# Kernel tuning notes

Hardware: AMD Instinct MI355X
Metric: run time of the kernel (lower is better)

## Reference

```python
import jax, jax.numpy as jnp
import numpy as np

HEAD_DIM = 64
K = 3              # kernel_size
DILATION = 1
SCALE = HEAD_DIM ** (-0.5)
PAD = DILATION * (K - 1) // 2


def setup_inputs() -> dict:
    key = jax.random.key(0)
    kq, kk, kv = jax.random.split(key, 3)
    shape = (8, 512, 56, 56)  # B, d, H, W
    return {
        "q": jax.random.normal(kq, shape, dtype=jnp.float32),
        "k": jax.random.normal(kk, shape, dtype=jnp.float32),
        "v": jax.random.normal(kv, shape, dtype=jnp.float32),
    }


def _unfold(x, B, h, H, W):
    # torch nn.Unfold(kernel=K, dilation=1, padding=PAD, stride=1):
    # output [B, d*K*K, H*W] with (channel, kh, kw) channel-major ordering,
    # which matches lax.conv_general_dilated_patches output layout.
    p = jax.lax.conv_general_dilated_patches(
        x, (K, K), (1, 1), ((PAD, PAD), (PAD, PAD)),
        rhs_dilation=(DILATION, DILATION),
        dimension_numbers=("NCHW", "OIHW", "NCHW"),
    )  # [B, d*K*K, H, W]
    return p.reshape(B, h, HEAD_DIM, K * K, H * W)


def reference(q, k, v):
    B, d, H, W = q.shape
    h = d // HEAD_DIM  # number of heads
    # q -> [B, h, HW, head_dim]
    qr = q.reshape(B, h, HEAD_DIM, H * W).transpose(0, 1, 3, 2)
    ku = _unfold(k, B, h, H, W)  # [B, h, hd, K*K, HW]
    vu = _unfold(v, B, h, H, W)  # [B, h, hd, K*K, HW]
    # per-pixel local attention over the K*K window
    attn = jnp.einsum("bhpc,bhckp->bhpk", qr, ku) * SCALE  # [B,h,HW,K*K]
    attn = jax.nn.softmax(attn, axis=-1)
    out = jnp.einsum("bhpk,bhckp->bhpc", attn, vu)  # [B,h,HW,hd]
    # -> [B, HW, h, hd] -> [B, H, W, d]
    return out.transpose(0, 2, 1, 3).reshape(B, H, W, d)
```

## Files before the change

kernel.cpp:

```cpp
#include <hip/hip_runtime.h>


namespace {

constexpr int HD = 64, HH = 56, WW = 56, HW = HH * WW;
constexpr int CS = HW, DTOT = 512;
constexpr float SCALE = 0.125f;
constexpr int NP   = HH / 2;
constexpr int TSTR = 36;

__device__ __forceinline__ float tapL(float v) {
  int i = __float_as_int(v);
  return __int_as_float(__builtin_amdgcn_update_dpp(i, i, 0x138, 0xF, 0xF, false));
}
__device__ __forceinline__ float tapR(float v) {
  int i = __float_as_int(v);
  return __int_as_float(__builtin_amdgcn_update_dpp(i, i, 0x130, 0xF, 0xF, false));
}

__global__ __launch_bounds__(64, 2)
void adda_fwd(const float* __restrict__ qg, const float* __restrict__ kg,
              const float* __restrict__ vg, float* __restrict__ outg) {
  __shared__ float tbuf[128 * TSTR];

  int wg = (int)blockIdx.x;
  const int nwg = (int)gridDim.x;
  if ((nwg & 7) == 0) wg = (wg & 7) * (nwg >> 3) + (wg >> 3);

  const int pair = wg % NP;
  const int bh   = wg / NP;
  const int l    = (int)threadIdx.x;
  const int y    = pair * 2;
  const int x    = l < WW ? l : WW - 1;

  const long base = (long)bh * HD * HW;
  const int gy0 = (y > 0) ? y - 1 : 0;
  const int gy3 = (y + 2 < HH) ? y + 2 : HH - 1;

  const float* __restrict__ qp0 = qg + base + (long)y * WW + x;
  const float* __restrict__ qp1 = qg + base + (long)(y + 1) * WW + x;
  const float* __restrict__ k0p = kg + base + (long)gy0 * WW + x;
  const float* __restrict__ k1p = kg + base + (long)y * WW + x;
  const float* __restrict__ k2p = kg + base + (long)(y + 1) * WW + x;
  const float* __restrict__ k3p = kg + base + (long)gy3 * WW + x;
  const float* __restrict__ v0p = vg + base + (long)gy0 * WW + x;
  const float* __restrict__ v1p = vg + base + (long)y * WW + x;
  const float* __restrict__ v2p = vg + base + (long)(y + 1) * WW + x;
  const float* __restrict__ v3p = vg + base + (long)gy3 * WW + x;

  float lg[18];
#pragma unroll
  for (int n = 0; n < 18; ++n) lg[n] = 0.f;

  float q0A[8], q1A[8], a0A[8], a1A[8], a2A[8], a3A[8];
  float q0B[8], q1B[8], a0B[8], a1B[8], a2B[8], a3B[8];

#define LOADK(S, cb)                                    \
  _Pragma("unroll") for (int i = 0; i < 8; ++i) {       \
    q0##S[i] = qp0[((cb) + i) * CS];                    \
    q1##S[i] = qp1[((cb) + i) * CS];                    \
    a0##S[i] = k0p[((cb) + i) * CS];                    \
    a1##S[i] = k1p[((cb) + i) * CS];                    \
    a2##S[i] = k2p[((cb) + i) * CS];                    \
    a3##S[i] = k3p[((cb) + i) * CS];                    \
  }
#define CONSK(S)                                        \
  _Pragma("unroll") for (int i = 0; i < 8; ++i) {       \
    const float t0l = tapL(a0##S[i]), t0r = tapR(a0##S[i]); \
    const float t1l = tapL(a1##S[i]), t1r = tapR(a1##S[i]); \
    const float t2l = tapL(a2##S[i]), t2r = tapR(a2##S[i]); \
    const float t3l = tapL(a3##S[i]), t3r = tapR(a3##S[i]); \
    const float q0 = q0##S[i], q1 = q1##S[i];           \
    lg[0]  = fmaf(q0, t0l,      lg[0]);                 \
    lg[1]  = fmaf(q0, a0##S[i], lg[1]);                 \
    lg[2]  = fmaf(q0, t0r,      lg[2]);                 \
    lg[3]  = fmaf(q0, t1l,      lg[3]);                 \
    lg[4]  = fmaf(q0, a1##S[i], lg[4]);                 \
    lg[5]  = fmaf(q0, t1r,      lg[5]);                 \
    lg[6]  = fmaf(q0, t2l,      lg[6]);                 \
    lg[7]  = fmaf(q0, a2##S[i], lg[7]);                 \
    lg[8]  = fmaf(q0, t2r,      lg[8]);                 \
    lg[9]  = fmaf(q1, t1l,      lg[9]);                 \
    lg[10] = fmaf(q1, a1##S[i], lg[10]);                \
    lg[11] = fmaf(q1, t1r,      lg[11]);                \
    lg[12] = fmaf(q1, t2l,      lg[12]);                \
    lg[13] = fmaf(q1, a2##S[i], lg[13]);                \
    lg[14] = fmaf(q1, t2r,      lg[14]);                \
    lg[15] = fmaf(q1, t3l,      lg[15]);                \
    lg[16] = fmaf(q1, a3##S[i], lg[16]);                \
    lg[17] = fmaf(q1, t3r,      lg[17]);                \
  }

  LOADK(A, 0);
  LOADK(B, 8);  CONSK(A);
  LOADK(A, 16); CONSK(B);
  LOADK(B, 24); CONSK(A);
  LOADK(A, 32); CONSK(B);
  LOADK(B, 40); CONSK(A);
  LOADK(A, 48); CONSK(B);
  LOADK(B, 56); CONSK(A);

  float b0A[8], b1A[8], b2A[8], b3A[8];
  float b0B[8], b1B[8], b2B[8], b3B[8];
#define LOADV(S, cb)                                    \
  _Pragma("unroll") for (int i = 0; i < 8; ++i) {       \
    b0##S[i] = v0p[((cb) + i) * CS];                    \
    b1##S[i] = v1p[((cb) + i) * CS];                    \
    b2##S[i] = v2p[((cb) + i) * CS];                    \
    b3##S[i] = v3p[((cb) + i) * CS];                    \
  }
  LOADV(A, 0);
  CONSK(B);

  const bool okl = x > 0, okr = x < WW - 1;
  const bool okt0 = y > 0;
  const bool okb1 = (y + 2) < HH;
  const bool ok[18] = {
    okt0 && okl, okt0, okt0 && okr,
    okl,         true, okr,
    okl,         true, okr,
    okl,         true, okr,
    okl,         true, okr,
    okb1 && okl, okb1, okb1 && okr};
  float w[18];
#pragma unroll
  for (int e = 0; e < 2; ++e) {
    float mx = 0.f;
#pragma unroll
    for (int n = 0; n < 9; ++n) {
      w[e * 9 + n] = ok[e * 9 + n] ? lg[e * 9 + n] * SCALE : 0.f;
      mx = fmaxf(mx, w[e * 9 + n]);
    }
    float sum = 0.f;
#pragma unroll
    for (int n = 0; n < 9; ++n) { w[e * 9 + n] = __expf(w[e * 9 + n] - mx); sum += w[e * 9 + n]; }
    const float inv = 1.f / sum;
#pragma unroll
    for (int n = 0; n < 9; ++n)
      w[e * 9 + n] = ok[e * 9 + n] ? w[e * 9 + n] * inv : 0.f;
  }

  float* __restrict__ ob =
      outg + ((long)(bh >> 3) * HW + (long)y * WW) * DTOT + (bh & 7) * HD;

#define CONSV(S, sl)                                    \
  {                                                     \
    float o0[8], o1[8];                                 \
    _Pragma("unroll") for (int i = 0; i < 8; ++i) {     \
      const float t0l = tapL(b0##S[i]), t0r = tapR(b0##S[i]); \
      const float t1l = tapL(b1##S[i]), t1r = tapR(b1##S[i]); \
      const float t2l = tapL(b2##S[i]), t2r = tapR(b2##S[i]); \
      const float t3l = tapL(b3##S[i]), t3r = tapR(b3##S[i]); \
      float a = w[0] * t0l;                             \
      a = fmaf(w[1], b0##S[i], a);                      \
      a = fmaf(w[2], t0r, a);                           \
      a = fmaf(w[3], t1l, a);                           \
      a = fmaf(w[4], b1##S[i], a);                      \
      a = fmaf(w[5], t1r, a);                           \
      a = fmaf(w[6], t2l, a);                           \
      a = fmaf(w[7], b2##S[i], a);                      \
      a = fmaf(w[8], t2r, a);                           \
      o0[i] = a;                                        \
      float c = w[9] * t1l;                             \
      c = fmaf(w[10], b1##S[i], c);                     \
      c = fmaf(w[11], t1r, c);                          \
      c = fmaf(w[12], t2l, c);                          \
      c = fmaf(w[13], b2##S[i], c);                     \
      c = fmaf(w[14], t2r, c);                          \
      c = fmaf(w[15], t3l, c);                          \
      c = fmaf(w[16], b3##S[i], c);                     \
      c = fmaf(w[17], t3r, c);                          \
      o1[i] = c;                                        \
    }                                                   \
    *(float4*)&tbuf[l * TSTR + (sl) * 8]            = make_float4(o0[0], o0[1], o0[2], o0[3]); \
    *(float4*)&tbuf[l * TSTR + (sl) * 8 + 4]        = make_float4(o0[4], o0[5], o0[6], o0[7]); \
    *(float4*)&tbuf[(64 + l) * TSTR + (sl) * 8]     = make_float4(o1[0], o1[1], o1[2], o1[3]); \
    *(float4*)&tbuf[(64 + l) * TSTR + (sl) * 8 + 4] = make_float4(o1[4], o1[5], o1[6], o1[7]); \
  }
#define READOUT(ch0)                                    \
  _Pragma("unroll") for (int r = 0; r < 14; ++r) {      \
    const int g = r * 64 + l;                           \
    const int pxl = g >> 3, slot = g & 7;               \
    const int lrow = pxl + ((pxl >= 56) ? 8 : 0);       \
    const float4 tv = *(const float4*)&tbuf[lrow * TSTR + slot * 4]; \
    *(float4*)(ob + (long)pxl * DTOT + (ch0) + slot * 4) = tv;      \
  }

  LOADV(B, 8);  CONSV(A, 0);
  LOADV(A, 16); CONSV(B, 1);
  LOADV(B, 24); CONSV(A, 2);
  LOADV(A, 32); CONSV(B, 3);
  LOADV(B, 40); READOUT(0);
  CONSV(A, 0);
  LOADV(A, 48); CONSV(B, 1);
  LOADV(B, 56); CONSV(A, 2);
                CONSV(B, 3);
  READOUT(32);

#undef LOADK
#undef CONSK
#undef LOADV
#undef CONSV
#undef READOUT
}

}

extern "C" void kernel_launch(void* const* d_in, const int* in_sizes, int n_in,
                              void* d_out, int out_size, void* d_ws, size_t ws_size,
                              hipStream_t stream) {
  const float* q = (const float*)d_in[0];
  const float* k = (const float*)d_in[1];
  const float* v = (const float*)d_in[2];
  float* out = (float*)d_out;

  const int BH = in_sizes[0] / (HD * HW);
  dim3 grid(BH * NP);
  adda_fwd<<<grid, 64, 0, stream>>>(q, k, v, out);
}
```

Before: 33.81 us.

## Switch to triple-buffered 4-channel load pipeline for K and V stages

Replaces the double-buffered 8-channel register pipeline with three 4-channel buffers, so two chunks of loads stay in flight while the third is consumed. This aims to hide global-load latency better at roughly the same register footprint. Stores to the LDS transpose buffer become one float4 per row per chunk. The risks are that the finer chunks add more wait points, and that the compiler's scheduling or register allocation changes at 2 waves per SIMD.

After: 33.60 us, median of 2. No clear change (-0.6%).

```diff
diff --git a/kernel.cpp b/kernel.cpp
--- a/kernel.cpp
+++ b/kernel.cpp
@@ -52,11 +52,12 @@
 #pragma unroll
   for (int n = 0; n < 18; ++n) lg[n] = 0.f;
 
-  float q0A[8], q1A[8], a0A[8], a1A[8], a2A[8], a3A[8];
-  float q0B[8], q1B[8], a0B[8], a1B[8], a2B[8], a3B[8];
+  float q0A[4], q1A[4], a0A[4], a1A[4], a2A[4], a3A[4];
+  float q0B[4], q1B[4], a0B[4], a1B[4], a2B[4], a3B[4];
+  float q0C[4], q1C[4], a0C[4], a1C[4], a2C[4], a3C[4];
 
 #define LOADK(S, cb)                                    \
-  _Pragma("unroll") for (int i = 0; i < 8; ++i) {       \
+  _Pragma("unroll") for (int i = 0; i < 4; ++i) {       \
     q0##S[i] = qp0[((cb) + i) * CS];                    \
     q1##S[i] = qp1[((cb) + i) * CS];                    \
     a0##S[i] = k0p[((cb) + i) * CS];                    \
@@ -65,7 +66,7 @@
     a3##S[i] = k3p[((cb) + i) * CS];                    \
   }
 #define CONSK(S)                                        \
-  _Pragma("unroll") for (int i = 0; i < 8; ++i) {       \
+  _Pragma("unroll") for (int i = 0; i < 4; ++i) {       \
     const float t0l = tapL(a0##S[i]), t0r = tapR(a0##S[i]); \
     const float t1l = tapL(a1##S[i]), t1r = tapR(a1##S[i]); \
     const float t2l = tapL(a2##S[i]), t2r = tapR(a2##S[i]); \
@@ -91,26 +92,34 @@
     lg[17] = fmaf(q1, t3r,      lg[17]);                \
   }
 
-  LOADK(A, 0);
-  LOADK(B, 8);  CONSK(A);
-  LOADK(A, 16); CONSK(B);
-  LOADK(B, 24); CONSK(A);
-  LOADK(A, 32); CONSK(B);
-  LOADK(B, 40); CONSK(A);
-  LOADK(A, 48); CONSK(B);
-  LOADK(B, 56); CONSK(A);
-
-  float b0A[8], b1A[8], b2A[8], b3A[8];
-  float b0B[8], b1B[8], b2B[8], b3B[8];
+  float b0A[4], b1A[4], b2A[4], b3A[4];
+  float b0B[4], b1B[4], b2B[4], b3B[4];
+  float b0C[4], b1C[4], b2C[4], b3C[4];
 #define LOADV(S, cb)                                    \
-  _Pragma("unroll") for (int i = 0; i < 8; ++i) {       \
+  _Pragma("unroll") for (int i = 0; i < 4; ++i) {       \
     b0##S[i] = v0p[((cb) + i) * CS];                    \
     b1##S[i] = v1p[((cb) + i) * CS];                    \
     b2##S[i] = v2p[((cb) + i) * CS];                    \
     b3##S[i] = v3p[((cb) + i) * CS];                    \
   }
-  LOADV(A, 0);
-  CONSK(B);
+
+  LOADK(A, 0); LOADK(B, 4); LOADK(C, 8);
+  CONSK(A); LOADK(A, 12);
+  CONSK(B); LOADK(B, 16);
+  CONSK(C); LOADK(C, 20);
+  CONSK(A); LOADK(A, 24);
+  CONSK(B); LOADK(B, 28);
+  CONSK(C); LOADK(C, 32);
+  CONSK(A); LOADK(A, 36);
+  CONSK(B); LOADK(B, 40);
+  CONSK(C); LOADK(C, 44);
+  CONSK(A); LOADK(A, 48);
+  CONSK(B); LOADK(B, 52);
+  CONSK(C); LOADK(C, 56);
+  CONSK(A); LOADK(A, 60);
+  CONSK(B); LOADV(A, 0);
+  CONSK(C); LOADV(B, 4);
+  CONSK(A); LOADV(C, 8);
 
   const bool okl = x > 0, okr = x < WW - 1;
   const bool okt0 = y > 0;
@@ -145,8 +154,8 @@
 
 #define CONSV(S, sl)                                    \
   {                                                     \
-    float o0[8], o1[8];                                 \
-    _Pragma("unroll") for (int i = 0; i < 8; ++i) {     \
+    float o0[4], o1[4];                                 \
+    _Pragma("unroll") for (int i = 0; i < 4; ++i) {     \
       const float t0l = tapL(b0##S[i]), t0r = tapR(b0##S[i]); \
       const float t1l = tapL(b1##S[i]), t1r = tapR(b1##S[i]); \
       const float t2l = tapL(b2##S[i]), t2r = tapR(b2##S[i]); \
@@ -172,10 +181,10 @@
       c = fmaf(w[17], t3r, c);                          \
       o1[i] = c;                                        \
     }                                                   \
-    *(float4*)&tbuf[l * TSTR + (sl) * 8]            = make_float4(o0[0], o0[1], o0[2], o0[3]); \
-    *(float4*)&tbuf[l * TSTR + (sl) * 8 + 4]        = make_float4(o0[4], o0[5], o0[6], o0[7]); \
-    *(float4*)&tbuf[(64 + l) * TSTR + (sl) * 8]     = make_float4(o1[0], o1[1], o1[2], o1[3]); \
-    *(float4*)&tbuf[(64 + l) * TSTR + (sl) * 8 + 4] = make_float4(o1[4], o1[5], o1[6], o1[7]); \
+    *(float4*)&tbuf[l * TSTR + (sl) * 4] =              \
+        make_float4(o0[0], o0[1], o0[2], o0[3]);        \
+    *(float4*)&tbuf[(64 + l) * TSTR + (sl) * 4] =       \
+        make_float4(o1[0], o1[1], o1[2], o1[3]);        \
   }
 #define READOUT(ch0)                                    \
   _Pragma("unroll") for (int r = 0; r < 14; ++r) {      \
@@ -186,15 +195,23 @@
     *(float4*)(ob + (long)pxl * DTOT + (ch0) + slot * 4) = tv;      \
   }
 
-  LOADV(B, 8);  CONSV(A, 0);
-  LOADV(A, 16); CONSV(B, 1);
-  LOADV(B, 24); CONSV(A, 2);
-  LOADV(A, 32); CONSV(B, 3);
-  LOADV(B, 40); READOUT(0);
-  CONSV(A, 0);
-  LOADV(A, 48); CONSV(B, 1);
-  LOADV(B, 56); CONSV(A, 2);
-                CONSV(B, 3);
+  CONSV(A, 0); LOADV(A, 12);
+  CONSV(B, 1); LOADV(B, 16);
+  CONSV(C, 2); LOADV(C, 20);
+  CONSV(A, 3); LOADV(A, 24);
+  CONSV(B, 4); LOADV(B, 28);
+  CONSV(C, 5); LOADV(C, 32);
+  CONSV(A, 6); LOADV(A, 36);
+  CONSV(B, 7); LOADV(B, 40);
+  READOUT(0);
+  CONSV(C, 0); LOADV(C, 44);
+  CONSV(A, 1); LOADV(A, 48);
+  CONSV(B, 2); LOADV(B, 52);
+  CONSV(C, 3); LOADV(C, 56);
+  CONSV(A, 4); LOADV(A, 60);
+  CONSV(B, 5);
+  CONSV(C, 6);
+  CONSV(A, 7);
   READOUT(32);
 
 #undef LOADK
```

## Split work across two waves: channel-split QK logits, row-split PV output

Applied to the files above, without the earlier changes.

Each workgroup now runs two wavefronts. For the logits, each wave accumulates partial dot products over half of the 64 channels and the halves are combined through shared memory with barriers. For the output, each wave handles one of the two output rows and loads only three V rows, which removes the duplicated second-row FMA chain per wave. This doubles thread-level parallelism and lowers per-wave register pressure, in exchange for an LDS reduction, two __syncthreads, and some redundant V row loads across the two waves.

Result: slower. 44.27 us (+30.9%).

```diff
diff --git a/kernel.cpp b/kernel.cpp
--- a/kernel.cpp
+++ b/kernel.cpp
@@ -18,10 +18,10 @@
   return __int_as_float(__builtin_amdgcn_update_dpp(i, i, 0x130, 0xF, 0xF, false));
 }
 
-__global__ __launch_bounds__(64, 2)
+__global__ __launch_bounds__(128, 4)
 void adda_fwd(const float* __restrict__ qg, const float* __restrict__ kg,
               const float* __restrict__ vg, float* __restrict__ outg) {
-  __shared__ float tbuf[128 * TSTR];
+  __shared__ float tbuf[2 * 64 * TSTR];
 
   int wg = (int)blockIdx.x;
   const int nwg = (int)gridDim.x;
@@ -29,24 +29,29 @@
 
   const int pair = wg % NP;
   const int bh   = wg / NP;
-  const int l    = (int)threadIdx.x;
+  const int l    = (int)threadIdx.x & 63;
+  const int wv   = (int)threadIdx.x >> 6;
   const int y    = pair * 2;
+  const int yr   = y + wv;
   const int x    = l < WW ? l : WW - 1;
 
-  const long base = (long)bh * HD * HW;
+  const long base  = (long)bh * HD * HW;
+  const long cbase = base + (long)(wv * 32) * CS;
   const int gy0 = (y > 0) ? y - 1 : 0;
   const int gy3 = (y + 2 < HH) ? y + 2 : HH - 1;
 
-  const float* __restrict__ qp0 = qg + base + (long)y * WW + x;
-  const float* __restrict__ qp1 = qg + base + (long)(y + 1) * WW + x;
-  const float* __restrict__ k0p = kg + base + (long)gy0 * WW + x;
-  const float* __restrict__ k1p = kg + base + (long)y * WW + x;
-  const float* __restrict__ k2p = kg + base + (long)(y + 1) * WW + x;
-  const float* __restrict__ k3p = kg + base + (long)gy3 * WW + x;
-  const float* __restrict__ v0p = vg + base + (long)gy0 * WW + x;
-  const float* __restrict__ v1p = vg + base + (long)y * WW + x;
-  const float* __restrict__ v2p = vg + base + (long)(y + 1) * WW + x;
-  const float* __restrict__ v3p = vg + base + (long)gy3 * WW + x;
+  const float* __restrict__ qp0 = qg + cbase + (long)y * WW + x;
+  const float* __restrict__ qp1 = qg + cbase + (long)(y + 1) * WW + x;
+  const float* __restrict__ k0p = kg + cbase + (long)gy0 * WW + x;
+  const float* __restrict__ k1p = kg + cbase + (long)y * WW + x;
+  const float* __restrict__ k2p = kg + cbase + (long)(y + 1) * WW + x;
+  const float* __restrict__ k3p = kg + cbase + (long)gy3 * WW + x;
+
+  const int vy0 = (yr > 0) ? yr - 1 : 0;
+  const int vy2 = (yr + 1 < HH) ? yr + 1 : HH - 1;
+  const float* __restrict__ v0p = vg + base + (long)vy0 * WW + x;
+  const float* __restrict__ v1p = vg + base + (long)yr * WW + x;
+  const float* __restrict__ v2p = vg + base + (long)vy2 * WW + x;
 
   float lg[18];
 #pragma unroll
@@ -91,66 +96,67 @@
     lg[17] = fmaf(q1, t3r,      lg[17]);                \
   }
 
-  LOADK(A, 0);
-  LOADK(B, 8);  CONSK(A);
-  LOADK(A, 16); CONSK(B);
-  LOADK(B, 24); CONSK(A);
-  LOADK(A, 32); CONSK(B);
-  LOADK(B, 40); CONSK(A);
-  LOADK(A, 48); CONSK(B);
-  LOADK(B, 56); CONSK(A);
-
-  float b0A[8], b1A[8], b2A[8], b3A[8];
-  float b0B[8], b1B[8], b2B[8], b3B[8];
+  float b0A[8], b1A[8], b2A[8];
+  float b0B[8], b1B[8], b2B[8];
 #define LOADV(S, cb)                                    \
   _Pragma("unroll") for (int i = 0; i < 8; ++i) {       \
     b0##S[i] = v0p[((cb) + i) * CS];                    \
     b1##S[i] = v1p[((cb) + i) * CS];                    \
     b2##S[i] = v2p[((cb) + i) * CS];                    \
-    b3##S[i] = v3p[((cb) + i) * CS];                    \
-  }
+  }
+
+  LOADK(A, 0);
+  LOADK(B, 8);  CONSK(A);
+  LOADK(A, 16); CONSK(B);
+  LOADK(B, 24); CONSK(A);
+                CONSK(B);
   LOADV(A, 0);
-  CONSK(B);
+  LOADV(B, 8);
+
+  {
+    float* outbox = &tbuf[wv * 2304];
+    const int src = wv ? 0 : 9;
+#pragma unroll
+    for (int n = 0; n < 9; ++n) outbox[n * 64 + l] = lg[src + n];
+  }
+  __syncthreads();
+  {
+    const float* inbox = &tbuf[(wv ^ 1) * 2304];
+    const int dst = wv ? 9 : 0;
+#pragma unroll
+    for (int n = 0; n < 9; ++n) lg[dst + n] += inbox[n * 64 + l];
+  }
+  __syncthreads();
 
   const bool okl = x > 0, okr = x < WW - 1;
-  const bool okt0 = y > 0;
-  const bool okb1 = (y + 2) < HH;
-  const bool ok[18] = {
-    okt0 && okl, okt0, okt0 && okr,
-    okl,         true, okr,
-    okl,         true, okr,
-    okl,         true, okr,
-    okl,         true, okr,
-    okb1 && okl, okb1, okb1 && okr};
-  float w[18];
-#pragma unroll
-  for (int e = 0; e < 2; ++e) {
-    float mx = 0.f;
-#pragma unroll
-    for (int n = 0; n < 9; ++n) {
-      w[e * 9 + n] = ok[e * 9 + n] ? lg[e * 9 + n] * SCALE : 0.f;
-      mx = fmaxf(mx, w[e * 9 + n]);
-    }
-    float sum = 0.f;
-#pragma unroll
-    for (int n = 0; n < 9; ++n) { w[e * 9 + n] = __expf(w[e * 9 + n] - mx); sum += w[e * 9 + n]; }
-    const float inv = 1.f / sum;
-#pragma unroll
-    for (int n = 0; n < 9; ++n)
-      w[e * 9 + n] = ok[e * 9 + n] ? w[e * 9 + n] * inv : 0.f;
-  }
-
+  const bool vt = wv ? true : (y > 0);
+  const bool vb = wv ? (y + 2 < HH) : true;
+  const bool ok[9] = {vt && okl, vt, vt && okr,
+                      okl,       true, okr,
+                      vb && okl, vb, vb && okr};
+  const int lo = wv * 9;
+  float w[9];
+  float mx = 0.f;
+#pragma unroll
+  for (int n = 0; n < 9; ++n) { w[n] = ok[n] ? lg[lo + n] * SCALE : 0.f; mx = fmaxf(mx, w[n]); }
+  float sum = 0.f;
+#pragma unroll
+  for (int n = 0; n < 9; ++n) { w[n] = __expf(w[n] - mx); sum += w[n]; }
+  const float inv = 1.f / sum;
+#pragma unroll
+  for (int n = 0; n < 9; ++n) w[n] = ok[n] ? w[n] * inv : 0.f;
+
+  float* __restrict__ tw = &tbuf[wv * 64 * TSTR];
   float* __restrict__ ob =
-      outg + ((long)(bh >> 3) * HW + (long)y * WW) * DTOT + (bh & 7) * HD;
+      outg + ((long)(bh >> 3) * HW + (long)yr * WW) * DTOT + (bh & 7) * HD;
 
 #define CONSV(S, sl)                                    \
   {                                                     \
-    float o0[8], o1[8];                                 \
+    float o[8];                                         \
     _Pragma("unroll") for (int i = 0; i < 8; ++i) {     \
       const float t0l = tapL(b0##S[i]), t0r = tapR(b0##S[i]); \
       const float t1l = tapL(b1##S[i]), t1r = tapR(b1##S[i]); \
       const float t2l = tapL(b2##S[i]), t2r = tapR(b2##S[i]); \
-      const float t3l = tapL(b3##S[i]), t3r = tapR(b3##S[i]); \
       float a = w[0] * t0l;                             \
       a = fmaf(w[1], b0##S[i], a);                      \
       a = fmaf(w[2], t0r, a);                           \
@@ -160,41 +166,28 @@
       a = fmaf(w[6], t2l, a);                           \
       a = fmaf(w[7], b2##S[i], a);                      \
       a = fmaf(w[8], t2r, a);                           \
-      o0[i] = a;                                        \
-      float c = w[9] * t1l;                             \
-      c = fmaf(w[10], b1##S[i], c);                     \
-      c = fmaf(w[11], t1r, c);                          \
-      c = fmaf(w[12], t2l, c);                          \
-      c = fmaf(w[13], b2##S[i], c);                     \
-      c = fmaf(w[14], t2r, c);                          \
-      c = fmaf(w[15], t3l, c);                          \
-      c = fmaf(w[16], b3##S[i], c);                     \
-      c = fmaf(w[17], t3r, c);                          \
-      o1[i] = c;                                        \
+      o[i] = a;                                         \
     }                                                   \
-    *(float4*)&tbuf[l * TSTR + (sl) * 8]            = make_float4(o0[0], o0[1], o0[2], o0[3]); \
-    *(float4*)&tbuf[l * TSTR + (sl) * 8 + 4]        = make_float4(o0[4], o0[5], o0[6], o0[7]); \
-    *(float4*)&tbuf[(64 + l) * TSTR + (sl) * 8]     = make_float4(o1[0], o1[1], o1[2], o1[3]); \
-    *(float4*)&tbuf[(64 + l) * TSTR + (sl) * 8 + 4] = make_float4(o1[4], o1[5], o1[6], o1[7]); \
+    *(float4*)&tw[l * TSTR + (sl) * 8]     = make_float4(o[0], o[1], o[2], o[3]); \
+    *(float4*)&tw[l * TSTR + (sl) * 8 + 4] = make_float4(o[4], o[5], o[6], o[7]); \
   }
 #define READOUT(ch0)                                    \
-  _Pragma("unroll") for (int r = 0; r < 14; ++r) {      \
+  _Pragma("unroll") for (int r = 0; r < 7; ++r) {       \
     const int g = r * 64 + l;                           \
     const int pxl = g >> 3, slot = g & 7;               \
-    const int lrow = pxl + ((pxl >= 56) ? 8 : 0);       \
-    const float4 tv = *(const float4*)&tbuf[lrow * TSTR + slot * 4]; \
-    *(float4*)(ob + (long)pxl * DTOT + (ch0) + slot * 4) = tv;      \
-  }
-
-  LOADV(B, 8);  CONSV(A, 0);
-  LOADV(A, 16); CONSV(B, 1);
-  LOADV(B, 24); CONSV(A, 2);
-  LOADV(A, 32); CONSV(B, 3);
-  LOADV(B, 40); READOUT(0);
-  CONSV(A, 0);
-  LOADV(A, 48); CONSV(B, 1);
-  LOADV(B, 56); CONSV(A, 2);
-                CONSV(B, 3);
+    const float4 tv = *(const float4*)&tw[pxl * TSTR + slot * 4]; \
+    *(float4*)(ob + (long)pxl * DTOT + (ch0) + slot * 4) = tv;    \
+  }
+
+  CONSV(A, 0); LOADV(A, 16);
+  CONSV(B, 1); LOADV(B, 24);
+  CONSV(A, 2); LOADV(A, 32);
+  CONSV(B, 3); LOADV(B, 40);
+  READOUT(0);
+  CONSV(A, 0); LOADV(A, 48);
+  CONSV(B, 1); LOADV(B, 56);
+  CONSV(A, 2);
+  CONSV(B, 3);
   READOUT(32);
 
 #undef LOADK
@@ -216,5 +209,5 @@
 
   const int BH = in_sizes[0] / (HD * HW);
   dim3 grid(BH * NP);
-  adda_fwd<<<grid, 64, 0, stream>>>(q, k, v, out);
-}
+  adda_fwd<<<grid, 128, 0, stream>>>(q, k, v, out);
+}
```
